# Kernel tuning notes

Measured on AMD Instinct MI355X. Metric: run time of the kernel, lower is better.

## Reference

```python
import jax, jax.numpy as jnp
import numpy as np
import itertools

ZOOM = 2.0  # zoom_factor per init_kwargs


def _interpn_linear(vol, locs):
    """vol: [*vol_shape, C]; locs: list of nb_dims float arrays of shape new_shape."""
    nb = len(locs)
    C = vol.shape[-1]
    max_loc = [vol.shape[d] - 1 for d in range(nb)]
    clipped = [jnp.clip(locs[d], 0.0, max_loc[d]) for d in range(nb)]
    loc0 = [jnp.clip(jnp.floor(locs[d]), 0.0, max_loc[d]) for d in range(nb)]
    loc1 = [jnp.clip(loc0[d] + 1.0, 0.0, max_loc[d]) for d in range(nb)]
    i0 = [x.astype(jnp.int32) for x in loc0]
    i1 = [x.astype(jnp.int32) for x in loc1]
    diff1 = [loc1[d] - clipped[d] for d in range(nb)]  # weight paired with corner 0
    diff0 = [1.0 - diff1[d] for d in range(nb)]        # weight paired with corner 1
    idxs = [i0, i1]
    wts = [diff1, diff0]
    volf = vol.reshape(-1, C)
    # column-major-style flattening per sub2ind: k = cumprod(reversed vol_shape)
    k = np.cumprod(np.array(vol.shape[:-1])[::-1])
    out = jnp.zeros(locs[0].shape + (C,), dtype=vol.dtype)
    for c in itertools.product([0, 1], repeat=nb):  # 2^nb corners (fixed, small)
        subs = [idxs[c[d]][d] for d in range(nb)]
        flat = subs[-1]
        for i, v in enumerate(subs[:-1][::-1]):
            flat = flat + v * int(k[i])
        val = volf[flat]  # gather -> [*new_shape, C]
        w = wts[c[0]][0]
        for d in range(1, nb):
            w = w * wts[c[d]][d]
        out = out + w[..., None] * val
    return out


def _resize_one(vol):
    """vol: [D,H,W,C] -> [2D,2H,2W,C] via linear interp at loc = grid/zoom."""
    nb = vol.ndim - 1
    new_shape = tuple(int(vol.shape[d] * ZOOM) for d in range(nb))
    grids = jnp.meshgrid(*[jnp.arange(n, dtype=jnp.float32) for n in new_shape],
                         indexing='ij')
    locs = [g / ZOOM for g in grids]  # grid + offset, offset = grid/zoom - grid
    return _interpn_linear(vol, locs)


def setup_inputs() -> dict:
    key = jax.random.key(0)
    vol = jax.random.normal(key, (2, 96, 96, 96, 2), dtype=jnp.float32)
    return {"vol": vol}


def reference(vol):
    return jax.vmap(_resize_one)(vol)  # [B, 192, 192, 192, 2]
```

## Files before the change

kernel.cpp:

```cpp
#include <hip/hip_runtime.h>

constexpr int NIN  = 96;
constexpr int NOUT = 192;
constexpr int TZ = 4, TY = 4;
constexpr int HZ = TZ + 1, HY = TY + 1, HX = NIN + 1;
constexpr int NT = NIN / TZ;

__global__ __launch_bounds__(256) void resize_zoom2_tiled(
        const float* __restrict__ in, float* __restrict__ out) {
    __shared__ float2 S[HZ * HY * HX];

    int bid = blockIdx.x;
    int yt = bid % NT;
    int t  = bid / NT;
    int zt = t % NT;
    int b  = t / NT;
    int z0 = zt * TZ, y0 = yt * TY;

    const float2* vin = (const float2*)in + (size_t)b * ((size_t)NIN * NIN * NIN);

    for (int i = threadIdx.x; i < HZ * HY * HX; i += 256) {
        int xx = i % HX;
        int r  = i / HX;
        int dy = r % HY;
        int dz = r / HY;
        int zi = min(z0 + dz, NIN - 1);
        int yi = min(y0 + dy, NIN - 1);
        int xi = min(xx, NIN - 1);
        S[i] = vin[((size_t)zi * NIN + yi) * NIN + xi];
    }
    __syncthreads();

    float4* vout = (float4*)out;
    int Zb = 2 * z0, Yb = 2 * y0;

    #pragma unroll 4
    for (int k = 0; k < 24; ++k) {
        int j  = threadIdx.x + k * 256;
        int xp = j % NIN;
        int r  = j / NIN;
        int yo = r & 7;
        int zo = r >> 3;
        int zA = zo >> 1, zB = zA + (zo & 1);
        int yA = yo >> 1, yB = yA + (yo & 1);
        const float2* rowAA = S + (zA * HY + yA) * HX;
        const float2* rowAB = S + (zA * HY + yB) * HX;
        const float2* rowBA = S + (zB * HY + yA) * HX;
        const float2* rowBB = S + (zB * HY + yB) * HX;
        float2 a0 = rowAA[xp],     a1 = rowAB[xp],     a2 = rowBA[xp],     a3 = rowBB[xp];
        float2 c0 = rowAA[xp + 1], c1 = rowAB[xp + 1], c2 = rowBA[xp + 1], c3 = rowBB[xp + 1];
        float sex = a0.x + a1.x + a2.x + a3.x;
        float sey = a0.y + a1.y + a2.y + a3.y;
        float sox = c0.x + c1.x + c2.x + c3.x;
        float soy = c0.y + c1.y + c2.y + c3.y;
        float4 v = make_float4(0.25f * sex, 0.25f * sey,
                               0.125f * (sex + sox), 0.125f * (sey + soy));
        size_t o4 = (((size_t)(b * NOUT + (Zb + zo))) * NOUT + (Yb + yo)) * (NOUT / 2) + xp;
        vout[o4] = v;
    }
}

extern "C" void kernel_launch(void* const* d_in, const int* in_sizes, int n_in,
                              void* d_out, int out_size, void* d_ws, size_t ws_size,
                              hipStream_t stream) {
    const float* in = (const float*)d_in[0];
    float* out = (float*)d_out;
    const int grid = 2 * NT * NT;
    resize_zoom2_tiled<<<grid, 256, 0, stream>>>(in, out);
}
```

Measured before the change: 124.7 us.

## Restructure resize kernel with z-sliding reuse, float4 halo loads, smaller tiles

The z tile shrinks to 2 and blocks drop to 192 threads, doubling the number of blocks. Each thread now owns one x column and walks down z, reusing the y-summed pair from the previous z row instead of re-reading four corners from LDS. The halo load uses float4 global reads plus a separate load for the clamped edge column. This is meant to cut LDS traffic and index arithmetic and to improve load vectorization, at the cost of a larger relative halo overhead per block.

```diff
diff --git a/kernel.cpp b/kernel.cpp
--- a/kernel.cpp
+++ b/kernel.cpp
@@ -1,62 +1,80 @@
 #include <hip/hip_runtime.h>
 
-constexpr int NIN  = 96;
-constexpr int NOUT = 192;
-constexpr int TZ = 4, TY = 4;
-constexpr int HZ = TZ + 1, HY = TY + 1, HX = NIN + 1;
-constexpr int NT = NIN / TZ;
+constexpr int NIN = 96, NOUT = 192;
+constexpr int TZ = 2, TY = 4;
+constexpr int HZ = TZ + 1, HY = TY + 1;
+constexpr int ROWS = HZ * HY;
+constexpr int HXP = 98;
+constexpr int F4R = NIN / 2;
+constexpr int NTZ = NIN / TZ, NTY = NIN / TY;
 
-__global__ __launch_bounds__(256) void resize_zoom2_tiled(
+__global__ __launch_bounds__(192) void resize_zoom2_v3(
         const float* __restrict__ in, float* __restrict__ out) {
-    __shared__ float2 S[HZ * HY * HX];
+    __shared__ __align__(16) float2 S[ROWS * HXP];
 
-    int bid = blockIdx.x;
-    int yt = bid % NT;
-    int t  = bid / NT;
-    int zt = t % NT;
-    int b  = t / NT;
-    int z0 = zt * TZ, y0 = yt * TY;
+    const int bid = blockIdx.x;
+    const int yt = bid % NTY;
+    const int tt = bid / NTY;
+    const int zt = tt % NTZ;
+    const int b  = tt / NTZ;
+    const int z0 = zt * TZ, y0 = yt * TY;
 
-    const float2* vin = (const float2*)in + (size_t)b * ((size_t)NIN * NIN * NIN);
+    const float* vb = in + (size_t)b * ((size_t)NIN * NIN * NIN * 2);
+    const float4* vin4 = (const float4*)vb;
 
-    for (int i = threadIdx.x; i < HZ * HY * HX; i += 256) {
-        int xx = i % HX;
-        int r  = i / HX;
-        int dy = r % HY;
-        int dz = r / HY;
-        int zi = min(z0 + dz, NIN - 1);
-        int yi = min(y0 + dy, NIN - 1);
-        int xi = min(xx, NIN - 1);
-        S[i] = vin[((size_t)zi * NIN + yi) * NIN + xi];
+    for (int i = threadIdx.x; i < ROWS * F4R; i += 192) {
+        int r = i / F4R, col = i - r * F4R;
+        int zi = min(z0 + r / HY, NIN - 1);
+        int yi = min(y0 + (r - (r / HY) * HY), NIN - 1);
+        float4 v = vin4[(size_t)(zi * NIN + yi) * F4R + col];
+        *(float4*)((float*)(S + r * HXP) + 4 * col) = v;
+    }
+    if (threadIdx.x < ROWS) {
+        int r = threadIdx.x;
+        int zi = min(z0 + r / HY, NIN - 1);
+        int yi = min(y0 + r % HY, NIN - 1);
+        S[r * HXP + NIN] = ((const float2*)vb)[(size_t)(zi * NIN + yi) * NIN + (NIN - 1)];
     }
     __syncthreads();
 
+    const int xp = threadIdx.x % NIN;
+    const int yh = threadIdx.x / NIN;
     float4* vout = (float4*)out;
-    int Zb = 2 * z0, Yb = 2 * y0;
+    constexpr size_t ZSTR = (size_t)NOUT * (NOUT / 2);
+    size_t ob = ((size_t)(b * NOUT + 2 * z0) * NOUT + (2 * y0 + yh)) * (NOUT / 2) + xp;
 
-    #pragma unroll 4
-    for (int k = 0; k < 24; ++k) {
-        int j  = threadIdx.x + k * 256;
-        int xp = j % NIN;
-        int r  = j / NIN;
-        int yo = r & 7;
-        int zo = r >> 3;
-        int zA = zo >> 1, zB = zA + (zo & 1);
-        int yA = yo >> 1, yB = yA + (yo & 1);
-        const float2* rowAA = S + (zA * HY + yA) * HX;
-        const float2* rowAB = S + (zA * HY + yB) * HX;
-        const float2* rowBA = S + (zB * HY + yA) * HX;
-        const float2* rowBB = S + (zB * HY + yB) * HX;
-        float2 a0 = rowAA[xp],     a1 = rowAB[xp],     a2 = rowBA[xp],     a3 = rowBB[xp];
-        float2 c0 = rowAA[xp + 1], c1 = rowAB[xp + 1], c2 = rowBA[xp + 1], c3 = rowBB[xp + 1];
-        float sex = a0.x + a1.x + a2.x + a3.x;
-        float sey = a0.y + a1.y + a2.y + a3.y;
-        float sox = c0.x + c1.x + c2.x + c3.x;
-        float soy = c0.y + c1.y + c2.y + c3.y;
-        float4 v = make_float4(0.25f * sex, 0.25f * sey,
-                               0.125f * (sex + sox), 0.125f * (sey + soy));
-        size_t o4 = (((size_t)(b * NOUT + (Zb + zo))) * NOUT + (Yb + yo)) * (NOUT / 2) + xp;
-        vout[o4] = v;
+    #pragma unroll
+    for (int y2 = 0; y2 < TY; ++y2) {
+        const int yo = 2 * y2 + yh;
+        const int yA = yo >> 1, yB = yA + (yo & 1);
+        const float2* pA = S + yA * HXP;
+        const float2* pB = S + yB * HXP;
+
+        float2 aA = pA[xp],     aB = pB[xp];
+        float2 cA = pA[xp + 1], cB = pB[xp + 1];
+        float sy_x  = aA.x + aB.x, sy_y  = aA.y + aB.y;
+        float syc_x = cA.x + cB.x, syc_y = cA.y + cB.y;
+        size_t o = ob + (size_t)y2 * NOUT;
+
+        #pragma unroll
+        for (int k = 0; k < TZ; ++k) {
+            const float2* qA = pA + (k + 1) * HY * HXP;
+            const float2* qB = pB + (k + 1) * HY * HXP;
+            float2 bA = qA[xp],     bB = qB[xp];
+            float2 dA = qA[xp + 1], dB = qB[xp + 1];
+            float ty_x  = bA.x + bB.x, ty_y  = bA.y + bB.y;
+            float tyc_x = dA.x + dB.x, tyc_y = dA.y + dB.y;
+
+            vout[o + (size_t)(2 * k) * ZSTR] =
+                make_float4(0.5f * sy_x, 0.5f * sy_y,
+                            0.25f * (sy_x + syc_x), 0.25f * (sy_y + syc_y));
+            float ux = sy_x + ty_x, uy = sy_y + ty_y;
+            float vx = ux + syc_x + tyc_x, vy = uy + syc_y + tyc_y;
+            vout[o + (size_t)(2 * k + 1) * ZSTR] =
+                make_float4(0.25f * ux, 0.25f * uy, 0.125f * vx, 0.125f * vy);
+
+            sy_x = ty_x; sy_y = ty_y; syc_x = tyc_x; syc_y = tyc_y;
+        }
     }
 }
 
@@ -65,6 +83,6 @@
                               hipStream_t stream) {
     const float* in = (const float*)d_in[0];
     float* out = (float*)d_out;
-    const int grid = 2 * NT * NT;
-    resize_zoom2_tiled<<<grid, 256, 0, stream>>>(in, out);
+    const int grid = 2 * NTZ * NTY;
+    resize_zoom2_v3<<<grid, 192, 0, stream>>>(in, out);
 }
```

Measured after the change: 122.9 us. No clear change (-1.5%).
